# Optimization experiments

Measured on AMD Instinct MI355X. Metric: run time of the kernel, lower is better.

Reference implementation:

```python
import jax, jax.numpy as jnp
import numpy as np

HEADS = 16
EPS = 1e-5  # torch LayerNorm default


def _ln(x, s, b):
    m = jnp.mean(x, axis=-1, keepdims=True)
    v = jnp.mean((x - m) ** 2, axis=-1, keepdims=True)
    return (x - m) * jax.lax.rsqrt(v + EPS) * s + b


def setup_inputs() -> dict:
    key = jax.random.key(0)
    B, N, D, DEPTH, MLP = 2, 1024, 1024, 6, 4096
    ks = jax.random.split(key, 6)
    s = 0.02  # init scale so activations stay well-conditioned
    return {
        "x": jax.random.normal(ks[0], (B, N, D), dtype=jnp.float32),
        "ln1_s": jnp.ones((DEPTH, D), jnp.float32),
        "ln1_b": jnp.zeros((DEPTH, D), jnp.float32),
        "w_qkv": jax.random.normal(ks[1], (DEPTH, D, 3 * D), dtype=jnp.float32) * s,
        "w_out": jax.random.normal(ks[2], (DEPTH, D, D), dtype=jnp.float32) * s,
        "b_out": jnp.zeros((DEPTH, D), jnp.float32),
        "ln2_s": jnp.ones((DEPTH, D), jnp.float32),
        "ln2_b": jnp.zeros((DEPTH, D), jnp.float32),
        "w1": jax.random.normal(ks[3], (DEPTH, D, MLP), dtype=jnp.float32) * s,
        "b1": jnp.zeros((DEPTH, MLP), jnp.float32),
        "w2": jax.random.normal(ks[4], (DEPTH, MLP, D), dtype=jnp.float32) * s,
        "b2": jnp.zeros((DEPTH, D), jnp.float32),
    }


def reference(x, ln1_s, ln1_b, w_qkv, w_out, b_out, ln2_s, ln2_b, w1, b1, w2, b2):
    D = x.shape[-1]
    dh = D // HEADS
    scale = D ** -0.5  # NOTE: original scales by full dim**-0.5, not head_dim

    def layer(xc, p):
        l1s, l1b, wq, wo, bo, l2s, l2b, W1, B1, W2, B2 = p
        h = _ln(xc, l1s, l1b)
        b, n, _ = h.shape
        qkv = (h @ wq).reshape(b, n, 3, HEADS, dh)  # 'b n (qkv h d)' split order
        q = qkv[:, :, 0].transpose(0, 2, 1, 3)  # bhnd
        k = qkv[:, :, 1].transpose(0, 2, 1, 3)
        v = qkv[:, :, 2].transpose(0, 2, 1, 3)
        dots = jnp.einsum('bhid,bhjd->bhij', q, k) * scale
        attn = jax.nn.softmax(dots, axis=-1)
        o = jnp.einsum('bhij,bhjd->bhid', attn, v)
        o = o.transpose(0, 2, 1, 3).reshape(b, n, D)
        xc = xc + (o @ wo + bo)  # Residual(PreNorm(Attention))
        h2 = _ln(xc, l2s, l2b)
        xc = xc + (jax.nn.gelu(h2 @ W1 + B1, approximate=False) @ W2 + B2)
        return xc, None

    x, _ = jax.lax.scan(layer, x, (ln1_s, ln1_b, w_qkv, w_out, b_out,
                                   ln2_s, ln2_b, w1, b1, w2, b2))
    return x
```

## Files before the change

### kernel.cpp

```cpp
#include <hip/hip_runtime.h>
#include <math.h>

typedef unsigned short ushort_t;
typedef __bf16 bf16x8 __attribute__((ext_vector_type(8)));
typedef float f32x4 __attribute__((ext_vector_type(4)));

#define HEADS 16

__device__ __forceinline__ ushort_t f2b(float f) {
    unsigned int u = __float_as_uint(f);
    unsigned int r = (u + 0x7FFFu + ((u >> 16) & 1u)) >> 16;
    return (ushort_t)r;
}

__device__ __forceinline__ void g2lds(const void* g, void* l) {
    __builtin_amdgcn_global_load_lds(
        (const __attribute__((address_space(1))) unsigned int*)g,
        (__attribute__((address_space(3))) unsigned int*)l, 16, 0, 0);
}

__global__ __launch_bounds__(256) void copy_kernel(const float* __restrict__ x,
                                                   float* __restrict__ y) {
    int i = blockIdx.x * 256 + threadIdx.x;
    ((float4*)y)[i] = ((const float4*)x)[i];
}

__global__ __launch_bounds__(256) void transpose_kernel(const float* __restrict__ W,
                                                        ushort_t* __restrict__ Wt,
                                                        int K, int N) {
    __shared__ ushort_t sT[64 * 72];
    const int t = threadIdx.x;
    const int k0 = blockIdx.y * 64;
    const int n0 = blockIdx.x * 64;
    const int kk = t >> 4;
    const int nc = (t & 15) * 4;
#pragma unroll
    for (int i = 0; i < 4; i++) {
        int k = kk + i * 16;
        float4 v = *(const float4*)(W + (size_t)(k0 + k) * N + n0 + nc);
        const float* vf = (const float*)&v;
#pragma unroll
        for (int j = 0; j < 4; j++) sT[(nc + j) * 72 + k] = f2b(vf[j]);
    }
    __syncthreads();
#pragma unroll
    for (int p = 0; p < 2; p++) {
        int u = t + p * 256;
        int n = u >> 3;
        int kc = (u & 7) * 8;
        *(uint4*)(Wt + (size_t)(n0 + n) * K + k0 + kc) = *(const uint4*)(sT + n * 72 + kc);
    }
}

__global__ __launch_bounds__(256) void ln_kernel(const float* __restrict__ x,
                                                 const float* __restrict__ s,
                                                 const float* __restrict__ b,
                                                 ushort_t* __restrict__ out) {
    int row = blockIdx.x;
    int t = threadIdx.x;
    const float* xr = x + (size_t)row * 1024;
    float4 xv = *(const float4*)(xr + t * 4);
    float sum = xv.x + xv.y + xv.z + xv.w;
    float sq = xv.x * xv.x + xv.y * xv.y + xv.z * xv.z + xv.w * xv.w;
#pragma unroll
    for (int m = 1; m < 64; m <<= 1) {
        sum += __shfl_xor(sum, m);
        sq += __shfl_xor(sq, m);
    }
    __shared__ float red[8];
    int wave = t >> 6, lane = t & 63;
    if (lane == 0) { red[wave] = sum; red[4 + wave] = sq; }
    __syncthreads();
    sum = red[0] + red[1] + red[2] + red[3];
    sq = red[4] + red[5] + red[6] + red[7];
    float mean = sum * (1.0f / 1024.0f);
    float var = sq * (1.0f / 1024.0f) - mean * mean;
    float inv = rsqrtf(var + 1e-5f);
    float4 sv = *(const float4*)(s + t * 4);
    float4 bv = *(const float4*)(b + t * 4);
    unsigned int lo = (unsigned int)f2b((xv.x - mean) * inv * sv.x + bv.x) |
                      ((unsigned int)f2b((xv.y - mean) * inv * sv.y + bv.y) << 16);
    unsigned int hi = (unsigned int)f2b((xv.z - mean) * inv * sv.z + bv.z) |
                      ((unsigned int)f2b((xv.w - mean) * inv * sv.w + bv.w) << 16);
    uint2 o;
    o.x = lo; o.y = hi;
    *(uint2*)(out + (size_t)row * 1024 + t * 4) = o;
}

template <int MODE>
__global__ __launch_bounds__(256) void gemm_bt_kernel(
    const ushort_t* __restrict__ A, const ushort_t* __restrict__ Bt,
    const float* __restrict__ bias, float* __restrict__ res,
    ushort_t* __restrict__ outb, ushort_t* __restrict__ qo,
    ushort_t* __restrict__ ko, ushort_t* __restrict__ vto, int K, int N, int Ks) {
    __shared__ __align__(16) ushort_t sA[128 * 32];
    __shared__ __align__(16) ushort_t sB[128 * 32];
    const int t = threadIdx.x;
    const int lane = t & 63;
    const int wave = t >> 6;
    const int l15 = lane & 15;
    const int quad = lane >> 4;
    const int wm = wave >> 1, wn = wave & 1;
    const int m0 = blockIdx.y * 128;
    const int n0 = blockIdx.x * 128;
    const int kbeg = blockIdx.z * Ks;

    f32x4 acc[4][4];
#pragma unroll
    for (int i = 0; i < 4; i++)
#pragma unroll
        for (int j = 0; j < 4; j++) acc[i][j] = (f32x4){0.f, 0.f, 0.f, 0.f};

    const int r0 = t >> 2, c8 = (t & 3) * 8;
    const ushort_t* gA0 = A + (size_t)(m0 + r0) * K + kbeg + c8;
    const ushort_t* gA1 = A + (size_t)(m0 + 64 + r0) * K + kbeg + c8;
    const ushort_t* gB0 = Bt + (size_t)(n0 + r0) * K + kbeg + c8;
    const ushort_t* gB1 = Bt + (size_t)(n0 + 64 + r0) * K + kbeg + c8;
    ushort_t* lA0 = sA + (wave * 64) * 8;
    ushort_t* lA1 = sA + (256 + wave * 64) * 8;
    ushort_t* lB0 = sB + (wave * 64) * 8;
    ushort_t* lB1 = sB + (256 + wave * 64) * 8;

    const int nkt = Ks >> 5;
    for (int kt = 0; kt < nkt; kt++) {
        const int ko_off = kt * 32;
        __syncthreads();
        g2lds(gA0 + ko_off, lA0);
        g2lds(gA1 + ko_off, lA1);
        g2lds(gB0 + ko_off, lB0);
        g2lds(gB1 + ko_off, lB1);
        __syncthreads();
        bf16x8 af[4], bf[4];
#pragma unroll
        for (int i = 0; i < 4; i++) {
            af[i] = *(const bf16x8*)(sA + ((wm * 64 + i * 16 + l15) * 4 + quad) * 8);
            bf[i] = *(const bf16x8*)(sB + ((wn * 64 + i * 16 + l15) * 4 + quad) * 8);
        }
#pragma unroll
        for (int mi = 0; mi < 4; mi++)
#pragma unroll
            for (int ni = 0; ni < 4; ni++)
                acc[mi][ni] = __builtin_amdgcn_mfma_f32_16x16x32_bf16(
                    af[mi], bf[ni], acc[mi][ni], 0, 0, 0);
    }
#pragma unroll
    for (int mi = 0; mi < 4; mi++) {
#pragma unroll
        for (int ni = 0; ni < 4; ni++) {
#pragma unroll
            for (int r = 0; r < 4; r++) {
                int mg = m0 + wm * 64 + mi * 16 + quad * 4 + r;
                int ng = n0 + wn * 64 + ni * 16 + l15;
                float c = acc[mi][ni][r];
                if (MODE == 1) {
                    size_t idx = (size_t)mg * N + ng;
                    float add = c + (kbeg == 0 ? bias[ng] : 0.f);
                    if (gridDim.z > 1)
                        atomicAdd(&res[idx], add);
                    else
                        res[idx] = res[idx] + add;
                } else if (MODE == 2) {
                    float vv = c + bias[ng];
                    float g = 0.5f * vv * (1.0f + erff(vv * 0.70710678118654752f));
                    outb[(size_t)mg * N + ng] = f2b(g);
                } else {
                    int qkv = ng >> 10;
                    int rem = ng & 1023;
                    int hh = rem >> 6;
                    int dd = rem & 63;
                    int bb = mg >> 10;
                    int seq = mg & 1023;
                    ushort_t val = f2b(c);
                    if (qkv == 0)
                        qo[((size_t)(bb * HEADS + hh) * 1024 + seq) * 64 + dd] = val;
                    else if (qkv == 1)
                        ko[((size_t)(bb * HEADS + hh) * 1024 + seq) * 64 + dd] = val;
                    else
                        vto[((size_t)(bb * HEADS + hh) * 64 + dd) * 1024 + seq] = val;
                }
            }
        }
    }
}

__global__ __launch_bounds__(256) void attn_kernel(const ushort_t* __restrict__ q,
                                                   const ushort_t* __restrict__ k,
                                                   const ushort_t* __restrict__ vt,
                                                   ushort_t* __restrict__ o) {
    __shared__ __align__(16) ushort_t sK[64 * 72];
    __shared__ __align__(16) ushort_t sV[64 * 72];
    __shared__ __align__(16) ushort_t sP[4 * 16 * 72];
    const int t = threadIdx.x;
    const int lane = t & 63;
    const int w = t >> 6;
    const int l15 = lane & 15;
    const int quad = lane >> 4;
    const int qt = blockIdx.x;
    const int bh = blockIdx.y;

    bf16x8 aq[2];
    const ushort_t* qbase = q + ((size_t)bh * 1024 + qt * 64 + w * 16 + l15) * 64;
    aq[0] = *(const bf16x8*)(qbase + quad * 8);
    aq[1] = *(const bf16x8*)(qbase + 32 + quad * 8);

    float m_old[4], l_sum[4];
    f32x4 oacc[4];
#pragma unroll
    for (int r = 0; r < 4; r++) { m_old[r] = -1e30f; l_sum[r] = 0.f; }
#pragma unroll
    for (int i = 0; i < 4; i++) oacc[i] = (f32x4){0.f, 0.f, 0.f, 0.f};

    const float scale = 0.03125f;

    for (int kt = 0; kt < 16; kt++) {
        __syncthreads();
#pragma unroll
        for (int p = 0; p < 2; p++) {
            int u = t + p * 256;
            int row = u >> 3, ch = u & 7;
            uint4 v = *(const uint4*)(k + ((size_t)bh * 1024 + kt * 64 + row) * 64 + ch * 8);
            *(uint4*)(sK + row * 72 + ch * 8) = v;
            uint4 v2 = *(const uint4*)(vt + ((size_t)bh * 64 + row) * 1024 + kt * 64 + ch * 8);
            *(uint4*)(sV + row * 72 + ch * 8) = v2;
        }
        __syncthreads();
        f32x4 s[4];
#pragma unroll
        for (int nt = 0; nt < 4; nt++) {
            f32x4 a = (f32x4){0.f, 0.f, 0.f, 0.f};
#pragma unroll
            for (int ks = 0; ks < 2; ks++) {
                bf16x8 bk = *(const bf16x8*)(sK + (nt * 16 + l15) * 72 + ks * 32 + quad * 8);
                a = __builtin_amdgcn_mfma_f32_16x16x32_bf16(aq[ks], bk, a, 0, 0, 0);
            }
            s[nt] = a * scale;
        }
        float alpha[4];
#pragma unroll
        for (int r = 0; r < 4; r++) {
            float mx = fmaxf(fmaxf(s[0][r], s[1][r]), fmaxf(s[2][r], s[3][r]));
#pragma unroll
            for (int msk = 1; msk < 16; msk <<= 1) mx = fmaxf(mx, __shfl_xor(mx, msk));
            float mnew = fmaxf(m_old[r], mx);
            alpha[r] = __expf(m_old[r] - mnew);
            float psum = 0.f;
#pragma unroll
            for (int nt = 0; nt < 4; nt++) {
                float p = __expf(s[nt][r] - mnew);
                s[nt][r] = p;
                psum += p;
            }
#pragma unroll
            for (int msk = 1; msk < 16; msk <<= 1) psum += __shfl_xor(psum, msk);
            l_sum[r] = l_sum[r] * alpha[r] + psum;
            m_old[r] = mnew;
        }
#pragma unroll
        for (int i = 0; i < 4; i++)
#pragma unroll
            for (int r = 0; r < 4; r++) oacc[i][r] *= alpha[r];
#pragma unroll
        for (int nt = 0; nt < 4; nt++)
#pragma unroll
            for (int r = 0; r < 4; r++)
                sP[w * 1152 + (quad * 4 + r) * 72 + nt * 16 + l15] = f2b(s[nt][r]);
        __syncthreads();
#pragma unroll
        for (int nt = 0; nt < 4; nt++) {
#pragma unroll
            for (int ks = 0; ks < 2; ks++) {
                bf16x8 ap = *(const bf16x8*)(sP + w * 1152 + l15 * 72 + ks * 32 + quad * 8);
                bf16x8 bv = *(const bf16x8*)(sV + (nt * 16 + l15) * 72 + ks * 32 + quad * 8);
                oacc[nt] = __builtin_amdgcn_mfma_f32_16x16x32_bf16(ap, bv, oacc[nt], 0, 0, 0);
            }
        }
    }
    int b = bh >> 4, hh = bh & 15;
#pragma unroll
    for (int nt = 0; nt < 4; nt++)
#pragma unroll
        for (int r = 0; r < 4; r++) {
            int row = qt * 64 + w * 16 + quad * 4 + r;
            float val = oacc[nt][r] / l_sum[r];
            o[((size_t)b * 1024 + row) * 1024 + hh * 64 + nt * 16 + l15] = f2b(val);
        }
}

extern "C" void kernel_launch(void* const* d_in, const int* in_sizes, int n_in,
                              void* d_out, int out_size, void* d_ws, size_t ws_size,
                              hipStream_t stream) {
    const float* x = (const float*)d_in[0];
    const float* ln1_s = (const float*)d_in[1];
    const float* ln1_b = (const float*)d_in[2];
    const float* w_qkv = (const float*)d_in[3];
    const float* w_out = (const float*)d_in[4];
    const float* b_out = (const float*)d_in[5];
    const float* ln2_s = (const float*)d_in[6];
    const float* ln2_b = (const float*)d_in[7];
    const float* w1 = (const float*)d_in[8];
    const float* b1 = (const float*)d_in[9];
    const float* w2 = (const float*)d_in[10];
    const float* b2 = (const float*)d_in[11];

    float* res = (float*)d_out;
    char* wsb = (char*)d_ws;
    const size_t MB = 1024 * 1024;
    ushort_t* h = (ushort_t*)(wsb + 0 * MB);
    ushort_t* qb = (ushort_t*)(wsb + 4 * MB);
    ushort_t* kb = (ushort_t*)(wsb + 8 * MB);
    ushort_t* vtb = (ushort_t*)(wsb + 12 * MB);
    ushort_t* ob = (ushort_t*)(wsb + 16 * MB);
    ushort_t* ub = (ushort_t*)(wsb + 4 * MB);
    ushort_t* wqkv_t = (ushort_t*)(wsb + 20 * MB);
    ushort_t* wo_t = (ushort_t*)(wsb + 26 * MB);
    ushort_t* w12_t = (ushort_t*)(wsb + 20 * MB);

    copy_kernel<<<2048, 256, 0, stream>>>(x, res);
    for (int l = 0; l < 6; l++) {
        transpose_kernel<<<dim3(48, 16), 256, 0, stream>>>(
            w_qkv + (size_t)l * 1024 * 3072, wqkv_t, 1024, 3072);
        transpose_kernel<<<dim3(16, 16), 256, 0, stream>>>(
            w_out + (size_t)l * 1024 * 1024, wo_t, 1024, 1024);
        ln_kernel<<<2048, 256, 0, stream>>>(res, ln1_s + l * 1024, ln1_b + l * 1024, h);
        gemm_bt_kernel<0><<<dim3(24, 16, 1), 256, 0, stream>>>(
            h, wqkv_t, nullptr, nullptr, nullptr, qb, kb, vtb, 1024, 3072, 1024);
        attn_kernel<<<dim3(16, 32), 256, 0, stream>>>(qb, kb, vtb, ob);
        gemm_bt_kernel<1><<<dim3(8, 16, 2), 256, 0, stream>>>(
            ob, wo_t, b_out + l * 1024, res, nullptr, nullptr, nullptr, nullptr,
            1024, 1024, 512);
        transpose_kernel<<<dim3(64, 16), 256, 0, stream>>>(
            w1 + (size_t)l * 1024 * 4096, w12_t, 1024, 4096);
        ln_kernel<<<2048, 256, 0, stream>>>(res, ln2_s + l * 1024, ln2_b + l * 1024, h);
        gemm_bt_kernel<2><<<dim3(32, 16, 1), 256, 0, stream>>>(
            h, w12_t, b1 + l * 4096, nullptr, ub, nullptr, nullptr, nullptr,
            1024, 4096, 1024);
        transpose_kernel<<<dim3(16, 64), 256, 0, stream>>>(
            w2 + (size_t)l * 4096 * 1024, w12_t, 4096, 1024);
        gemm_bt_kernel<1><<<dim3(8, 16, 4), 256, 0, stream>>>(
            ub, w12_t, b2 + l * 1024, res, nullptr, nullptr, nullptr, nullptr,
            4096, 1024, 1024);
    }
}
```

Before: 1.703 ms.

## Double GEMM K-tile to 64 with XOR-swizzled LDS layout and more split-K

The bf16 MFMA GEMM now stages a 64-wide K slice per iteration instead of 32, so there are half as many barrier pairs per K. Rows are stored 64 elements wide with an XOR swizzle on 16-byte chunks to avoid LDS bank conflicts on the fragment reads. The out-projection GEMM moves from split-K 2 to split-K 4 to fill more CUs. In exchange, LDS use per block doubles, which may lower occupancy, and the extra split adds atomics on the residual.

```diff
diff --git a/kernel.cpp b/kernel.cpp
--- a/kernel.cpp
+++ b/kernel.cpp
@@ -93,8 +93,8 @@
     const float* __restrict__ bias, float* __restrict__ res,
     ushort_t* __restrict__ outb, ushort_t* __restrict__ qo,
     ushort_t* __restrict__ ko, ushort_t* __restrict__ vto, int K, int N, int Ks) {
-    __shared__ __align__(16) ushort_t sA[128 * 32];
-    __shared__ __align__(16) ushort_t sB[128 * 32];
+    __shared__ __align__(16) ushort_t sA[128 * 64];
+    __shared__ __align__(16) ushort_t sB[128 * 64];
     const int t = threadIdx.x;
     const int lane = t & 63;
     const int wave = t >> 6;
@@ -111,37 +111,41 @@
 #pragma unroll
         for (int j = 0; j < 4; j++) acc[i][j] = (f32x4){0.f, 0.f, 0.f, 0.f};
 
-    const int r0 = t >> 2, c8 = (t & 3) * 8;
-    const ushort_t* gA0 = A + (size_t)(m0 + r0) * K + kbeg + c8;
-    const ushort_t* gA1 = A + (size_t)(m0 + 64 + r0) * K + kbeg + c8;
-    const ushort_t* gB0 = Bt + (size_t)(n0 + r0) * K + kbeg + c8;
-    const ushort_t* gB1 = Bt + (size_t)(n0 + 64 + r0) * K + kbeg + c8;
-    ushort_t* lA0 = sA + (wave * 64) * 8;
-    ushort_t* lA1 = sA + (256 + wave * 64) * 8;
-    ushort_t* lB0 = sB + (wave * 64) * 8;
-    ushort_t* lB1 = sB + (256 + wave * 64) * 8;
-
-    const int nkt = Ks >> 5;
+    const int rlow = lane >> 3;
+    const int chunk = (lane & 7) ^ rlow;
+    const int rowS = wave * 8 + rlow;
+    const ushort_t* gA = A + (size_t)(m0 + rowS) * K + kbeg + chunk * 8;
+    const ushort_t* gB = Bt + (size_t)(n0 + rowS) * K + kbeg + chunk * 8;
+    ushort_t* lA = sA + wave * 64 * 8;
+    ushort_t* lB = sB + wave * 64 * 8;
+    const int xorv = l15 & 7;
+
+    const int nkt = Ks >> 6;
     for (int kt = 0; kt < nkt; kt++) {
-        const int ko_off = kt * 32;
-        __syncthreads();
-        g2lds(gA0 + ko_off, lA0);
-        g2lds(gA1 + ko_off, lA1);
-        g2lds(gB0 + ko_off, lB0);
-        g2lds(gB1 + ko_off, lB1);
-        __syncthreads();
-        bf16x8 af[4], bf[4];
-#pragma unroll
-        for (int i = 0; i < 4; i++) {
-            af[i] = *(const bf16x8*)(sA + ((wm * 64 + i * 16 + l15) * 4 + quad) * 8);
-            bf[i] = *(const bf16x8*)(sB + ((wn * 64 + i * 16 + l15) * 4 + quad) * 8);
-        }
-#pragma unroll
-        for (int mi = 0; mi < 4; mi++)
-#pragma unroll
-            for (int ni = 0; ni < 4; ni++)
-                acc[mi][ni] = __builtin_amdgcn_mfma_f32_16x16x32_bf16(
-                    af[mi], bf[ni], acc[mi][ni], 0, 0, 0);
+        const size_t koff = (size_t)kt * 64;
+        __syncthreads();
+#pragma unroll
+        for (int p = 0; p < 4; p++) {
+            g2lds(gA + (size_t)p * 32 * K + koff, lA + p * 2048);
+            g2lds(gB + (size_t)p * 32 * K + koff, lB + p * 2048);
+        }
+        __syncthreads();
+#pragma unroll
+        for (int ks = 0; ks < 2; ks++) {
+            const int co = ((ks * 4 + quad) ^ xorv) * 8;
+            bf16x8 af[4], bf[4];
+#pragma unroll
+            for (int i = 0; i < 4; i++) {
+                af[i] = *(const bf16x8*)(sA + (wm * 64 + i * 16 + l15) * 64 + co);
+                bf[i] = *(const bf16x8*)(sB + (wn * 64 + i * 16 + l15) * 64 + co);
+            }
+#pragma unroll
+            for (int mi = 0; mi < 4; mi++)
+#pragma unroll
+                for (int ni = 0; ni < 4; ni++)
+                    acc[mi][ni] = __builtin_amdgcn_mfma_f32_16x16x32_bf16(
+                        af[mi], bf[ni], acc[mi][ni], 0, 0, 0);
+        }
     }
 #pragma unroll
     for (int mi = 0; mi < 4; mi++) {
@@ -325,9 +329,9 @@
         gemm_bt_kernel<0><<<dim3(24, 16, 1), 256, 0, stream>>>(
             h, wqkv_t, nullptr, nullptr, nullptr, qb, kb, vtb, 1024, 3072, 1024);
         attn_kernel<<<dim3(16, 32), 256, 0, stream>>>(qb, kb, vtb, ob);
-        gemm_bt_kernel<1><<<dim3(8, 16, 2), 256, 0, stream>>>(
+        gemm_bt_kernel<1><<<dim3(8, 16, 4), 256, 0, stream>>>(
             ob, wo_t, b_out + l * 1024, res, nullptr, nullptr, nullptr, nullptr,
-            1024, 1024, 512);
+            1024, 1024, 256);
         transpose_kernel<<<dim3(64, 16), 256, 0, stream>>>(
             w1 + (size_t)l * 1024 * 4096, w12_t, 1024, 4096);
         ln_kernel<<<2048, 256, 0, stream>>>(res, ln2_s + l * 1024, ln2_b + l * 1024, h);
```

Measured after the change: 1.616 ms. -5.1%, faster.
